# Optimization experiments

Measured on AMD Instinct MI355X. Metric: run time of the kernel, lower is better.

## Reference

```python
import jax, jax.numpy as jnp
import numpy as np

KERNEL = (9, 9, 9)  # box-filter window
KSIZE = KERNEL[0] * KERNEL[1] * KERNEL[2]  # 729
GAMMA = 1.0


def _box_sum(x):
    # x: [B, C, D, H, W] -> channel-sum then 9x9x9 sliding-window sum (SAME pad),
    # exactly matching F.conv3d with an all-ones [1, C, 9,9,9] kernel, pad=4.
    s = jnp.sum(x, axis=1, keepdims=True)  # [B,1,D,H,W]
    return jax.lax.reduce_window(
        s, jnp.asarray(0.0, s.dtype), jax.lax.add,
        window_dimensions=(1, 1) + KERNEL,
        window_strides=(1, 1, 1, 1, 1),
        padding='SAME')


def setup_inputs() -> dict:
    key = jax.random.key(0)
    k1, k2, k3 = jax.random.split(key, 3)
    shape = (2, 1, 160, 160, 160)
    return {
        'input': jax.random.normal(k1, shape, dtype=jnp.float32),
        'target': jax.random.normal(k2, shape, dtype=jnp.float32),
        'flow': jax.random.normal(k3, shape, dtype=jnp.float32),
    }


def reference(input, target, flow):
    # normalize target from (-1, 1) to (0, 1)
    target = (target + 1.0) * 0.5
    w = jax.nn.sigmoid(flow) ** GAMMA  # voxel-wise confidence weight

    T_sum = _box_sum(target)
    I_sum = _box_sum(input)
    TT_sum = _box_sum(target * target)
    II_sum = _box_sum(input * input)
    IT_sum = _box_sum(input * target)

    Ihat = I_sum / KSIZE
    That = T_sum / KSIZE
    cross = IT_sum - Ihat * T_sum - That * I_sum + That * Ihat * KSIZE
    T_var = TT_sum - 2.0 * That * T_sum + That * That * KSIZE
    I_var = II_sum - 2.0 * Ihat * I_sum + Ihat * Ihat * KSIZE

    cc = cross * cross * w / (T_var * I_var + 1e-5)
    return -1.0 * jnp.mean(cc)
```

## Files before the change

kernel.cpp:

```cpp
#include <hip/hip_runtime.h>


constexpr int NB = 2;
constexpr int ND = 160;
constexpr int NH = 160;
constexpr int NW = 160;
constexpr int TH = 16;
constexpr int TW = 16;
constexpr int DCHUNK = 32;
constexpr int NDCH = ND / DCHUNK;
constexpr int NPL = DCHUNK + 8;
constexpr int NIT = NPL + 2;
constexpr int TRS = 20;
constexpr int TFS = 24 * TRS + 8;
constexpr int PRS = 20;
constexpr int PFS = 16 * PRS + 8;
constexpr float INV_K = 1.0f / 729.0f;
constexpr double INV_COUNT = 1.0 / (double(NB) * ND * NH * NW);

__device__ __forceinline__ void issue_load(
    const float* __restrict__ in, const float* __restrict__ tg,
    int b, int dp, int h0, int w0, int tid,
    float4& iv, float4& tv)
{
    iv = make_float4(0.f, 0.f, 0.f, 0.f);
    tv = make_float4(0.f, 0.f, 0.f, 0.f);
    if (tid < 144 && ((unsigned)dp < (unsigned)ND)) {
        int r = tid / 6;
        int q = tid - r * 6;
        int gh = h0 - 4 + r;
        int gw = w0 - 4 + q * 4;
        if (((unsigned)gh < (unsigned)NH) && ((unsigned)gw < (unsigned)NW)) {
            int base = ((b * ND + dp) * NH + gh) * NW + gw;
            iv = *reinterpret_cast<const float4*>(in + base);
            float4 rv = *reinterpret_cast<const float4*>(tg + base);
            tv.x = fmaf(rv.x, 0.5f, 0.5f);
            tv.y = fmaf(rv.y, 0.5f, 0.5f);
            tv.z = fmaf(rv.z, 0.5f, 0.5f);
            tv.w = fmaf(rv.w, 0.5f, 0.5f);
        }
    }
}

__device__ __forceinline__ void stage(int tid, const float4& iv, const float4& tv,
                                      float* __restrict__ inT, float* __restrict__ tgT)
{
    if (tid < 144) {
        reinterpret_cast<float4*>(inT)[tid] = iv;
        reinterpret_cast<float4*>(tgT)[tid] = tv;
    }
}

#define W9SLIDE(EXPR, FI)                                                  \
    {                                                                      \
        float p0 = (EXPR(0)), p1 = (EXPR(1)), p2 = (EXPR(2)),              \
              p3 = (EXPR(3)), p4 = (EXPR(4)), p5 = (EXPR(5)),              \
              p6 = (EXPR(6)), p7 = (EXPR(7)), p8 = (EXPR(8)),              \
              p9 = (EXPR(9)), p10 = (EXPR(10)), p11 = (EXPR(11));          \
        float s = p0 + p1 + p2 + p3 + p4 + p5 + p6 + p7 + p8;              \
        float4 o;                                                          \
        o.x = s; s += p9 - p0;                                             \
        o.y = s; s += p10 - p1;                                            \
        o.z = s; s += p11 - p2;                                            \
        o.w = s;                                                           \
        *reinterpret_cast<float4*>(outp + (FI) * TFS) = o;                 \
    }

__device__ __forceinline__ void step2q(int tid, const float* __restrict__ inT,
                                       const float* __restrict__ tgT,
                                       float* __restrict__ t5)
{
    if (tid < 96) {
        const int r = tid >> 2, q = tid & 3;
        const float4* ip = reinterpret_cast<const float4*>(inT + r * 24 + 4 * q);
        const float4* tp = reinterpret_cast<const float4*>(tgT + r * 24 + 4 * q);
        const float4 i0 = ip[0], i1 = ip[1], i2 = ip[2];
        const float4 t0 = tp[0], t1 = tp[1], t2 = tp[2];
        const float ia[12] = {i0.x, i0.y, i0.z, i0.w, i1.x, i1.y, i1.z, i1.w,
                              i2.x, i2.y, i2.z, i2.w};
        const float ta[12] = {t0.x, t0.y, t0.z, t0.w, t1.x, t1.y, t1.z, t1.w,
                              t2.x, t2.y, t2.z, t2.w};
        float* outp = t5 + r * TRS + 4 * q;
        #define E_T(j)  ta[j]
        #define E_I(j)  ia[j]
        #define E_TT(j) (ta[j] * ta[j])
        #define E_II(j) (ia[j] * ia[j])
        #define E_IT(j) (ia[j] * ta[j])
        W9SLIDE(E_T, 0)
        W9SLIDE(E_I, 1)
        W9SLIDE(E_TT, 2)
        W9SLIDE(E_II, 3)
        W9SLIDE(E_IT, 4)
        #undef E_T
        #undef E_I
        #undef E_TT
        #undef E_II
        #undef E_IT
    }
}

__device__ __forceinline__ void hpass(int tid, const float* __restrict__ t5,
                                      float* __restrict__ Pb)
{
    if (tid < 80) {
        const int f = tid >> 4;
        const int rem = tid & 15;
        const int wq = rem >> 2, hs = rem & 3;
        const float* bp = t5 + f * TFS + hs * 4 * TRS + wq * 4;
        float4 r4[12];
        #pragma unroll
        for (int k = 0; k < 12; ++k)
            r4[k] = *reinterpret_cast<const float4*>(bp + k * TRS);
        float sx = r4[0].x, sy = r4[0].y, sz = r4[0].z, sw = r4[0].w;
        #pragma unroll
        for (int k = 1; k < 9; ++k) {
            sx += r4[k].x; sy += r4[k].y; sz += r4[k].z; sw += r4[k].w;
        }
        float* op = Pb + f * PFS + hs * 4 * PRS + wq * 4;
        *reinterpret_cast<float4*>(op) = make_float4(sx, sy, sz, sw);
        #pragma unroll
        for (int j = 1; j < 4; ++j) {
            sx += r4[8 + j].x - r4[j - 1].x;
            sy += r4[8 + j].y - r4[j - 1].y;
            sz += r4[8 + j].z - r4[j - 1].z;
            sw += r4[8 + j].w - r4[j - 1].w;
            *reinterpret_cast<float4*>(op + j * PRS) = make_float4(sx, sy, sz, sw);
        }
    }
}

__device__ __forceinline__ float cc_value(const float S[5], float flv)
{
    float wgt = 1.0f / (1.0f + __expf(-flv));
    float Ts = S[0], Is = S[1], TTs = S[2], IIs = S[3], ITs = S[4];
    float Ihat = Is * INV_K;
    float That = Ts * INV_K;
    float cross = ITs - Ihat * Ts - That * Is + That * Ihat * 729.0f;
    float T_var = TTs - 2.0f * That * Ts + That * That * 729.0f;
    float I_var = IIs - 2.0f * Ihat * Is + Ihat * Ihat * 729.0f;
    return cross * cross * wgt / (T_var * I_var + 1e-5f);
}

__global__ void __launch_bounds__(256, 4)
cc3d_main(const float* __restrict__ in, const float* __restrict__ tg,
          const float* __restrict__ fl, double* __restrict__ acc_out)
{
    __shared__ __align__(16) float inT[24 * 24];
    __shared__ __align__(16) float tgT[24 * 24];
    __shared__ __align__(16) float tmp5[2][5 * TFS];
    __shared__ __align__(16) float Pb[5 * PFS];
    __shared__ float red[4];

    const int tid = threadIdx.x;
    const int w0 = blockIdx.x * TW;
    const int h0 = blockIdx.y * TH;
    const int bz = blockIdx.z;
    const int b  = bz / NDCH;
    const int d0 = (bz - b * NDCH) * DCHUNK;
    const int hh = tid >> 4, ww = tid & 15;

    float ring[45];
    #pragma unroll
    for (int i = 0; i < 45; ++i) ring[i] = 0.f;
    float S[5] = {0.f, 0.f, 0.f, 0.f, 0.f};
    float acc = 0.f;
    float flv = 0.f, flv_next = 0.f;

    float4 civ, ctv;
    issue_load(in, tg, b, d0 - 4, h0, w0, tid, civ, ctv);

    for (int lb = 0; lb < 45; lb += 9) {
        #pragma unroll
        for (int li = 0; li < 9; ++li) {
            const int l = lb + li;
            if (l < NIT) {
                if (l >= 2) {
                    const int lm2 = l - 2;
                    const int dpz = d0 - 4 + lm2;
                    const bool vz = ((unsigned)dpz < (unsigned)ND);
                    const int slot = (li + 7) % 9;
                    #pragma unroll
                    for (int f = 0; f < 5; ++f) {
                        float pn = vz ? Pb[f * PFS + hh * PRS + ww] : 0.f;
                        S[f] += pn - ring[f * 9 + slot];
                        ring[f * 9 + slot] = pn;
                    }
                    if (lm2 >= 8) acc += cc_value(S, flv);
                }
                if (l < NPL) stage(tid, civ, ctv, inT, tgT);
                __syncthreads();
                if (l < NPL) {
                    const int dpl = d0 - 4 + l;
                    if ((unsigned)dpl < (unsigned)ND)
                        step2q(tid, inT, tgT, tmp5[l & 1]);
                }
                if (l >= 1 && l <= NPL) {
                    const int dph = d0 - 4 + (l - 1);
                    if ((unsigned)dph < (unsigned)ND)
                        hpass(tid, tmp5[(l - 1) & 1], Pb);
                }
                float4 niv = make_float4(0.f, 0.f, 0.f, 0.f), ntv = niv;
                if (l + 1 < NPL)
                    issue_load(in, tg, b, d0 - 4 + (l + 1), h0, w0, tid, niv, ntv);
                if (l >= 9 && l <= 40) {
                    int dout = d0 + (l - 9);
                    flv_next = fl[((b * ND + dout) * NH + (h0 + hh)) * NW + (w0 + ww)];
                }
                __syncthreads();
                civ = niv; ctv = ntv; flv = flv_next;
            }
        }
    }

    #pragma unroll
    for (int off = 32; off > 0; off >>= 1) acc += __shfl_down(acc, off);
    if ((tid & 63) == 0) red[tid >> 6] = acc;
    __syncthreads();
    if (tid == 0) {
        double v = (double)red[0] + (double)red[1] + (double)red[2] + (double)red[3];
        atomicAdd(acc_out, v);
    }
}

__global__ void cc3d_finalize(const double* __restrict__ acc, float* __restrict__ out)
{
    out[0] = (float)(-(acc[0] * INV_COUNT));
}

extern "C" void kernel_launch(void* const* d_in, const int* in_sizes, int n_in,
                              void* d_out, int out_size, void* d_ws, size_t ws_size,
                              hipStream_t stream)
{
    const float* in = (const float*)d_in[0];
    const float* tg = (const float*)d_in[1];
    const float* fl = (const float*)d_in[2];
    float* out = (float*)d_out;
    double* acc = (double*)d_ws;

    hipMemsetAsync(d_ws, 0, sizeof(double), stream);

    dim3 grid(NW / TW, NH / TH, NB * NDCH);
    cc3d_main<<<grid, dim3(256), 0, stream>>>(in, tg, fl, acc);
    cc3d_finalize<<<1, 1, 0, stream>>>(acc, out);
}
```

Baseline: 176.5 us.

## Pipeline stage/step2q/hpass across warps with double-buffered shared memory, one barrier

Restructures the per-plane loop into a software pipeline. Staging, the W-pass (step2q), the H-pass (hpass) and the D-ring update now run on different planes in the same iteration, assigned to disjoint thread groups: threads 96-239 stage, 0-95 run step2q and 176-255 run hpass. Input tiles and the Pb buffer are double-buffered so one __syncthreads per plane replaces two, at the cost of one extra pipeline iteration and more shared memory. Shared-memory padding constants (TFS, PRS) are also retuned.

Result: faster. 171.9 us (-2.6%).

```diff
diff --git a/kernel.cpp b/kernel.cpp
--- a/kernel.cpp
+++ b/kernel.cpp
@@ -10,24 +10,24 @@
 constexpr int DCHUNK = 32;
 constexpr int NDCH = ND / DCHUNK;
 constexpr int NPL = DCHUNK + 8;
-constexpr int NIT = NPL + 2;
+constexpr int NIT = NPL + 3;
 constexpr int TRS = 20;
-constexpr int TFS = 24 * TRS + 8;
-constexpr int PRS = 20;
+constexpr int TFS = 24 * TRS + 4;
+constexpr int PRS = 16;
 constexpr int PFS = 16 * PRS + 8;
 constexpr float INV_K = 1.0f / 729.0f;
 constexpr double INV_COUNT = 1.0 / (double(NB) * ND * NH * NW);
 
 __device__ __forceinline__ void issue_load(
     const float* __restrict__ in, const float* __restrict__ tg,
-    int b, int dp, int h0, int w0, int tid,
+    int b, int dp, int h0, int w0, int idx,
     float4& iv, float4& tv)
 {
     iv = make_float4(0.f, 0.f, 0.f, 0.f);
     tv = make_float4(0.f, 0.f, 0.f, 0.f);
-    if (tid < 144 && ((unsigned)dp < (unsigned)ND)) {
-        int r = tid / 6;
-        int q = tid - r * 6;
+    if ((unsigned)idx < 144u && ((unsigned)dp < (unsigned)ND)) {
+        int r = idx / 6;
+        int q = idx - r * 6;
         int gh = h0 - 4 + r;
         int gw = w0 - 4 + q * 4;
         if (((unsigned)gh < (unsigned)NH) && ((unsigned)gw < (unsigned)NW)) {
@@ -39,15 +39,6 @@
             tv.z = fmaf(rv.z, 0.5f, 0.5f);
             tv.w = fmaf(rv.w, 0.5f, 0.5f);
         }
-    }
-}
-
-__device__ __forceinline__ void stage(int tid, const float4& iv, const float4& tv,
-                                      float* __restrict__ inT, float* __restrict__ tgT)
-{
-    if (tid < 144) {
-        reinterpret_cast<float4*>(inT)[tid] = iv;
-        reinterpret_cast<float4*>(tgT)[tid] = tv;
     }
 }
 
@@ -70,62 +61,58 @@
                                        const float* __restrict__ tgT,
                                        float* __restrict__ t5)
 {
-    if (tid < 96) {
-        const int r = tid >> 2, q = tid & 3;
-        const float4* ip = reinterpret_cast<const float4*>(inT + r * 24 + 4 * q);
-        const float4* tp = reinterpret_cast<const float4*>(tgT + r * 24 + 4 * q);
-        const float4 i0 = ip[0], i1 = ip[1], i2 = ip[2];
-        const float4 t0 = tp[0], t1 = tp[1], t2 = tp[2];
-        const float ia[12] = {i0.x, i0.y, i0.z, i0.w, i1.x, i1.y, i1.z, i1.w,
-                              i2.x, i2.y, i2.z, i2.w};
-        const float ta[12] = {t0.x, t0.y, t0.z, t0.w, t1.x, t1.y, t1.z, t1.w,
-                              t2.x, t2.y, t2.z, t2.w};
-        float* outp = t5 + r * TRS + 4 * q;
-        #define E_T(j)  ta[j]
-        #define E_I(j)  ia[j]
-        #define E_TT(j) (ta[j] * ta[j])
-        #define E_II(j) (ia[j] * ia[j])
-        #define E_IT(j) (ia[j] * ta[j])
-        W9SLIDE(E_T, 0)
-        W9SLIDE(E_I, 1)
-        W9SLIDE(E_TT, 2)
-        W9SLIDE(E_II, 3)
-        W9SLIDE(E_IT, 4)
-        #undef E_T
-        #undef E_I
-        #undef E_TT
-        #undef E_II
-        #undef E_IT
-    }
-}
-
-__device__ __forceinline__ void hpass(int tid, const float* __restrict__ t5,
+    const int r = tid >> 2, q = tid & 3;
+    const float4* ip = reinterpret_cast<const float4*>(inT + r * 24 + 4 * q);
+    const float4* tp = reinterpret_cast<const float4*>(tgT + r * 24 + 4 * q);
+    const float4 i0 = ip[0], i1 = ip[1], i2 = ip[2];
+    const float4 t0 = tp[0], t1 = tp[1], t2 = tp[2];
+    const float ia[12] = {i0.x, i0.y, i0.z, i0.w, i1.x, i1.y, i1.z, i1.w,
+                          i2.x, i2.y, i2.z, i2.w};
+    const float ta[12] = {t0.x, t0.y, t0.z, t0.w, t1.x, t1.y, t1.z, t1.w,
+                          t2.x, t2.y, t2.z, t2.w};
+    float* outp = t5 + r * TRS + 4 * q;
+    #define E_T(j)  ta[j]
+    #define E_I(j)  ia[j]
+    #define E_TT(j) (ta[j] * ta[j])
+    #define E_II(j) (ia[j] * ia[j])
+    #define E_IT(j) (ia[j] * ta[j])
+    W9SLIDE(E_T, 0)
+    W9SLIDE(E_I, 1)
+    W9SLIDE(E_TT, 2)
+    W9SLIDE(E_II, 3)
+    W9SLIDE(E_IT, 4)
+    #undef E_T
+    #undef E_I
+    #undef E_TT
+    #undef E_II
+    #undef E_IT
+}
+
+__device__ __forceinline__ void hpass(int t, const float* __restrict__ t5,
                                       float* __restrict__ Pb)
 {
-    if (tid < 80) {
-        const int f = tid >> 4;
-        const int rem = tid & 15;
-        const int wq = rem >> 2, hs = rem & 3;
-        const float* bp = t5 + f * TFS + hs * 4 * TRS + wq * 4;
-        float4 r4[12];
-        #pragma unroll
-        for (int k = 0; k < 12; ++k)
-            r4[k] = *reinterpret_cast<const float4*>(bp + k * TRS);
-        float sx = r4[0].x, sy = r4[0].y, sz = r4[0].z, sw = r4[0].w;
-        #pragma unroll
-        for (int k = 1; k < 9; ++k) {
-            sx += r4[k].x; sy += r4[k].y; sz += r4[k].z; sw += r4[k].w;
-        }
-        float* op = Pb + f * PFS + hs * 4 * PRS + wq * 4;
-        *reinterpret_cast<float4*>(op) = make_float4(sx, sy, sz, sw);
-        #pragma unroll
-        for (int j = 1; j < 4; ++j) {
-            sx += r4[8 + j].x - r4[j - 1].x;
-            sy += r4[8 + j].y - r4[j - 1].y;
-            sz += r4[8 + j].z - r4[j - 1].z;
-            sw += r4[8 + j].w - r4[j - 1].w;
-            *reinterpret_cast<float4*>(op + j * PRS) = make_float4(sx, sy, sz, sw);
-        }
+    const int f = t >> 4;
+    const int rem = t & 15;
+    const int wq = rem >> 2, hs = rem & 3;
+    const float* bp = t5 + f * TFS + hs * 4 * TRS + wq * 4;
+    float4 r4[12];
+    #pragma unroll
+    for (int k = 0; k < 12; ++k)
+        r4[k] = *reinterpret_cast<const float4*>(bp + k * TRS);
+    float sx = r4[0].x, sy = r4[0].y, sz = r4[0].z, sw = r4[0].w;
+    #pragma unroll
+    for (int k = 1; k < 9; ++k) {
+        sx += r4[k].x; sy += r4[k].y; sz += r4[k].z; sw += r4[k].w;
+    }
+    float* op = Pb + f * PFS + hs * 4 * PRS + wq * 4;
+    *reinterpret_cast<float4*>(op) = make_float4(sx, sy, sz, sw);
+    #pragma unroll
+    for (int j = 1; j < 4; ++j) {
+        sx += r4[8 + j].x - r4[j - 1].x;
+        sy += r4[8 + j].y - r4[j - 1].y;
+        sz += r4[8 + j].z - r4[j - 1].z;
+        sw += r4[8 + j].w - r4[j - 1].w;
+        *reinterpret_cast<float4*>(op + j * PRS) = make_float4(sx, sy, sz, sw);
     }
 }
 
@@ -145,10 +132,10 @@
 cc3d_main(const float* __restrict__ in, const float* __restrict__ tg,
           const float* __restrict__ fl, double* __restrict__ acc_out)
 {
-    __shared__ __align__(16) float inT[24 * 24];
-    __shared__ __align__(16) float tgT[24 * 24];
+    __shared__ __align__(16) float inT[2][24 * 24];
+    __shared__ __align__(16) float tgT[2][24 * 24];
     __shared__ __align__(16) float tmp5[2][5 * TFS];
-    __shared__ __align__(16) float Pb[5 * PFS];
+    __shared__ __align__(16) float Pb[2][5 * PFS];
     __shared__ float red[4];
 
     const int tid = threadIdx.x;
@@ -158,6 +145,7 @@
     const int b  = bz / NDCH;
     const int d0 = (bz - b * NDCH) * DCHUNK;
     const int hh = tid >> 4, ww = tid & 15;
+    const int sidx = tid - 96;
 
     float ring[45];
     #pragma unroll
@@ -167,43 +155,50 @@
     float flv = 0.f, flv_next = 0.f;
 
     float4 civ, ctv;
-    issue_load(in, tg, b, d0 - 4, h0, w0, tid, civ, ctv);
-
-    for (int lb = 0; lb < 45; lb += 9) {
+    issue_load(in, tg, b, d0 - 4, h0, w0, sidx, civ, ctv);
+
+    for (int lb = 0; lb < NIT; lb += 9) {
         #pragma unroll
         for (int li = 0; li < 9; ++li) {
             const int l = lb + li;
             if (l < NIT) {
-                if (l >= 2) {
-                    const int lm2 = l - 2;
-                    const int dpz = d0 - 4 + lm2;
-                    const bool vz = ((unsigned)dpz < (unsigned)ND);
-                    const int slot = (li + 7) % 9;
+                if (l < NPL) {
+                    const int dpS = d0 - 4 + l;
+                    if (((unsigned)dpS < (unsigned)ND) && (unsigned)sidx < 144u) {
+                        reinterpret_cast<float4*>(inT[l & 1])[sidx] = civ;
+                        reinterpret_cast<float4*>(tgT[l & 1])[sidx] = ctv;
+                    }
+                }
+                if (l >= 1 && l <= NPL) {
+                    const int dp1 = d0 - 5 + l;
+                    if (((unsigned)dp1 < (unsigned)ND) && tid < 96)
+                        step2q(tid, inT[(l - 1) & 1], tgT[(l - 1) & 1],
+                               tmp5[(l - 1) & 1]);
+                }
+                if (l >= 2 && l <= NPL + 1) {
+                    const int dp2 = d0 - 6 + l;
+                    if (((unsigned)dp2 < (unsigned)ND) && tid >= 176)
+                        hpass(tid - 176, tmp5[l & 1], Pb[l & 1]);
+                }
+                if (l >= 3) {
+                    const int lm3 = l - 3;
+                    const int dp3 = d0 - 7 + l;
+                    const bool vz = ((unsigned)dp3 < (unsigned)ND);
+                    const int slot = (li + 6) % 9;
+                    const float* pb = Pb[(l + 1) & 1];
                     #pragma unroll
                     for (int f = 0; f < 5; ++f) {
-                        float pn = vz ? Pb[f * PFS + hh * PRS + ww] : 0.f;
+                        float pn = vz ? pb[f * PFS + hh * PRS + ww] : 0.f;
                         S[f] += pn - ring[f * 9 + slot];
                         ring[f * 9 + slot] = pn;
                     }
-                    if (lm2 >= 8) acc += cc_value(S, flv);
-                }
-                if (l < NPL) stage(tid, civ, ctv, inT, tgT);
-                __syncthreads();
-                if (l < NPL) {
-                    const int dpl = d0 - 4 + l;
-                    if ((unsigned)dpl < (unsigned)ND)
-                        step2q(tid, inT, tgT, tmp5[l & 1]);
-                }
-                if (l >= 1 && l <= NPL) {
-                    const int dph = d0 - 4 + (l - 1);
-                    if ((unsigned)dph < (unsigned)ND)
-                        hpass(tid, tmp5[(l - 1) & 1], Pb);
+                    if (lm3 >= 8) acc += cc_value(S, flv);
                 }
                 float4 niv = make_float4(0.f, 0.f, 0.f, 0.f), ntv = niv;
                 if (l + 1 < NPL)
-                    issue_load(in, tg, b, d0 - 4 + (l + 1), h0, w0, tid, niv, ntv);
-                if (l >= 9 && l <= 40) {
-                    int dout = d0 + (l - 9);
+                    issue_load(in, tg, b, d0 - 3 + l, h0, w0, sidx, niv, ntv);
+                if (l >= 10 && l <= 41) {
+                    int dout = d0 + l - 10;
                     flv_next = fl[((b * ND + dout) * NH + (h0 + hh)) * NW + (w0 + ww)];
                 }
                 __syncthreads();
```
